# Optimization experiments

Hardware: AMD Instinct MI355X
Metric: run time of the kernel (lower is better)

## Reference

```python
import jax, jax.numpy as jnp
import numpy as np

B, T = 256, 800
D_IN, H, L, V = 128, 512, 2, 128


def setup_inputs() -> dict:
    key = jax.random.key(0)
    ks = jax.random.split(key, 12)
    s = 0.1  # init scale for stability
    return {
        "W_ih0": jax.random.normal(ks[0], (4 * H, D_IN), jnp.float32) * s,
        "W_hh0": jax.random.normal(ks[1], (4 * H, H), jnp.float32) * s,
        "b_ih0": jax.random.normal(ks[2], (4 * H,), jnp.float32) * s,
        "b_hh0": jax.random.normal(ks[3], (4 * H,), jnp.float32) * s,
        "W_ih1": jax.random.normal(ks[4], (4 * H, H), jnp.float32) * s,
        "W_hh1": jax.random.normal(ks[5], (4 * H, H), jnp.float32) * s,
        "b_ih1": jax.random.normal(ks[6], (4 * H,), jnp.float32) * s,
        "b_hh1": jax.random.normal(ks[7], (4 * H,), jnp.float32) * s,
        "W_lin": jax.random.normal(ks[8], (V, H), jnp.float32) * s,
        "b_lin": jax.random.normal(ks[9], (V,), jnp.float32) * s,
        "z": jax.random.randint(ks[10], (B, T), 0, V, jnp.int32),
        "num_frames": jax.random.randint(ks[11], (B,), 100, 800, jnp.int32),
    }


def _lstm_log_prob(layers, W_lin, b_lin, z, num_frames):
    # teacher-forced inputs: step i sees one_hot(z[:, i-1]), zeros at i=0
    oh = jax.nn.one_hot(z[:, :-1], D_IN, dtype=jnp.float32)          # [B, T-1, D]
    inputs = jnp.concatenate([jnp.zeros((B, 1, D_IN), jnp.float32), oh], axis=1)
    inputs = jnp.transpose(inputs, (1, 0, 2))                         # [T, B, D]

    def step(carry, x_t):
        h, c = carry  # each [L, B, H]
        inp = x_t
        hs, cs = [], []
        for l, (Wih, Whh, bih, bhh) in enumerate(layers):
            gates = inp @ Wih.T + h[l] @ Whh.T + bih + bhh            # [B, 4H]
            i, f, g, o = jnp.split(gates, 4, axis=-1)                 # torch gate order i,f,g,o
            c_new = jax.nn.sigmoid(f) * c[l] + jax.nn.sigmoid(i) * jnp.tanh(g)
            h_new = jax.nn.sigmoid(o) * jnp.tanh(c_new)
            hs.append(h_new)
            cs.append(c_new)
            inp = h_new
        logits_t = inp @ W_lin.T + b_lin                              # [B, V]
        return (jnp.stack(hs), jnp.stack(cs)), logits_t

    h0 = jnp.zeros((L, B, H), jnp.float32)
    c0 = jnp.zeros((L, B, H), jnp.float32)
    _, logits = jax.lax.scan(step, (h0, c0), inputs)                  # [T, B, V]
    logits = jnp.transpose(logits, (1, 0, 2))                         # [B, T, V]

    logp = jax.nn.log_softmax(logits, axis=-1)
    nll = -jnp.take_along_axis(logp, z[..., None].astype(jnp.int32), axis=-1)[..., 0]  # [B, T]
    mask = (jnp.arange(T)[None, :] < num_frames[:, None]).astype(nll.dtype)
    return (nll * mask).mean(axis=-1)                                 # [B] (mean over full T, as in torch)


def reference(W_ih0, W_hh0, b_ih0, b_hh0, W_ih1, W_hh1, b_ih1, b_hh1, W_lin, b_lin, z, num_frames):
    layers = [(W_ih0, W_hh0, b_ih0, b_hh0), (W_ih1, W_hh1, b_ih1, b_hh1)]
    return _lstm_log_prob(layers, W_lin, b_lin, z, num_frames)
```

## Files before the change

### kernel.cpp

```cpp
#include <hip/hip_runtime.h>

#define TT 800

typedef __attribute__((ext_vector_type(8))) short bf16x8;
typedef __attribute__((ext_vector_type(4))) float f32x4;
typedef unsigned short u16;
typedef unsigned int u32;
typedef unsigned long long u64;

constexpr int NCW = 128, NWG = 136, RT = 32;
constexpr size_t WL0A_OFF = 0;
constexpr size_t WL0B_OFF = 2097152;
constexpr size_t WL1_OFF  = 2621440;
constexpr size_t WLIN_OFF = 6815744;
constexpr size_t H0_OFF   = 6946816;
constexpr size_t H1_OFF   = 7471104;
constexpr size_t BAR_OFF  = 7995392;
constexpr int HB = 256 * 512;
constexpr int A_ST = 520;
constexpr int G_OFF_B = 33280;
constexpr int P_OFF_B = 49792;
constexpr int LDS_BYTES = 53248;

__device__ __forceinline__ u16 f2b(float x) {
  u32 u = __float_as_uint(x);
  return (u16)((u + 0x7FFFu + ((u >> 16) & 1u)) >> 16);
}
__device__ __forceinline__ float b2f(u16 v) { return __uint_as_float(((u32)v) << 16); }
__device__ __forceinline__ float sigf(float x) { return 1.f / (1.f + __expf(-x)); }
__device__ __forceinline__ float tanh_f(float x) { float e = __expf(2.f * x); return 1.f - 2.f / (e + 1.f); }

__device__ __forceinline__ u64 ld_coh8(const u64* p) {
  return __hip_atomic_load(p, __ATOMIC_RELAXED, __HIP_MEMORY_SCOPE_AGENT);
}
__device__ __forceinline__ void st_coh8(u64* p, u64 v) {
  __hip_atomic_store(p, v, __ATOMIC_RELAXED, __HIP_MEMORY_SCOPE_AGENT);
}
__device__ __forceinline__ void fpost_l(u32* fw, u32 v) {
  *(volatile u32*)fw = v;
}
__device__ __forceinline__ void fpost_a(u32* fw, u32 v) {
  __hip_atomic_store(fw, v, __ATOMIC_RELAXED, __HIP_MEMORY_SCOPE_AGENT);
}
__device__ __forceinline__ void wave_poll(u32* Fw, int lane, u32 thr, bool lok) {
  int idx = (lane < 17) ? lane : 16;
  if (lok) {
    while (true) {
      u32 v = *(volatile u32*)(Fw + idx);
      if (__all((int)(v >= thr))) break;
      asm volatile("buffer_inv" ::: "memory");
    }
  } else {
    while (true) {
      u32 v = __hip_atomic_load(Fw + idx, __ATOMIC_RELAXED, __HIP_MEMORY_SCOPE_AGENT);
      if (__all((int)(v >= thr))) break;
      __builtin_amdgcn_s_sleep(1);
    }
  }
}
__device__ __forceinline__ void l1inv() { asm volatile("buffer_inv" ::: "memory"); }

__global__ void prep_kernel(const float* __restrict__ wih0, const float* __restrict__ whh0,
                            const float* __restrict__ wih1, const float* __restrict__ whh1,
                            const float* __restrict__ wlinf,
                            u16* __restrict__ wl0a, u16* __restrict__ wl0b,
                            u16* __restrict__ wl1, u16* __restrict__ wlin) {
  int i = blockIdx.x * 256 + threadIdx.x;
  const int NA = 2048 * 512, NB = 128 * 2048, N1 = 2048 * 1024, N2 = 128 * 512;
  if (i < NA) {
    int col = i >> 9, k = i & 511;
    wl0a[i] = f2b(whh0[col * 512 + k]);
  } else if (i < NA + NB) {
    int j = i - NA, k = j >> 11, col = j & 2047;
    wl0b[j] = f2b(wih0[col * 128 + k]);
  } else if (i < NA + NB + N1) {
    int j = i - NA - NB, col = j >> 10, k = j & 1023;
    float v = (k < 512) ? wih1[col * 512 + k] : whh1[col * 512 + (k - 512)];
    wl1[j] = f2b(v);
  } else if (i < NA + NB + N1 + N2) {
    int j = i - NA - NB - N1, col = j >> 9, k = j & 511;
    wlin[j] = f2b(wlinf[col * 512 + k]);
  }
}

__global__ __launch_bounds__(256, 1) void lstm_kernel(
    const float* __restrict__ bih0, const float* __restrict__ bhh0,
    const float* __restrict__ bih1, const float* __restrict__ bhh1,
    const float* __restrict__ blin,
    const int* __restrict__ z, const int* __restrict__ nfr,
    const u16* __restrict__ wl0a, const u16* __restrict__ wl0b,
    const u16* __restrict__ wl1, const u16* __restrict__ wlin,
    u16* __restrict__ h0buf, u16* __restrict__ h1buf,
    u32* __restrict__ bars, float* __restrict__ out) {
  extern __shared__ char smem[];
  u16* A = (u16*)smem;
  float* Gf = (float*)(smem + G_OFF_B);
  float* Pm = (float*)(smem + P_OFF_B);
  float* Ps = Pm + 256;
  float* Pt = Ps + 256;
  const int wg = blockIdx.x;
  const int w_all = wg >> 3;
  const bool isC = (w_all < 16);
  const int tile = wg & 7;
  const int w = isC ? w_all : 16;
  const int slot = isC ? w : 16;
  const int tid = threadIdx.x, lane = tid & 63, wv = tid >> 6;
  const int l15 = lane & 15, l4 = lane >> 4;
  const int row0 = tile * RT;
  u32* Fw = bars + tile * 32;
  const f32x4 VZ = {0.f, 0.f, 0.f, 0.f};
  const int rC = tid >> 3, u0C = (tid & 7) * 4;
  const int cuL = tid & 31, rgL = tid >> 5;

  float c0s[4] = {0, 0, 0, 0}, c1s[4] = {0, 0, 0, 0};
  float accN = 0.f, nflv = 0.f;
  float bias0c[2], bias1c[2], biasLc[2];
  bf16x8 bq0R[32];
  bf16x8 bq1R[64];
  bf16x8 wlR[32];

  if (isC) {
#pragma unroll
    for (int cb = 0; cb < 2; ++cb) {
      int col = wv * 512 + w * 32 + cb * 16 + l15;
      bias0c[cb] = bih0[col] + bhh0[col];
      bias1c[cb] = bih1[col] + bhh1[col];
      const u16* b0 = wl0a + (size_t)col * 512 + l4 * 8;
#pragma unroll
      for (int kb = 0; kb < 16; ++kb) bq0R[cb * 16 + kb] = *(const bf16x8*)(b0 + kb * 32);
      const u16* b1 = wl1 + (size_t)col * 1024 + l4 * 8;
#pragma unroll
      for (int kb = 0; kb < 32; ++kb) bq1R[cb * 32 + kb] = *(const bf16x8*)(b1 + kb * 32);
    }
  } else {
#pragma unroll
    for (int cb = 0; cb < 2; ++cb) {
      int colV = wv * 32 + cb * 16 + l15;
      biasLc[cb] = blin[colV];
      const u16* bL = wlin + (size_t)colV * 512 + l4 * 8;
#pragma unroll
      for (int kb = 0; kb < 16; ++kb) wlR[cb * 16 + kb] = *(const bf16x8*)(bL + kb * 32);
    }
    if (rgL == 0) nflv = (float)nfr[row0 + cuL];
  }

  u32 xcc;
  asm volatile("s_getreg_b32 %0, hwreg(HW_REG_XCC_ID)" : "=s"(xcc));
  {
    int* hls = (int*)Pm;
    if (tid == 0) {
      u32 bit = 1u << (xcc & 31u);
      __hip_atomic_fetch_or(bars + 256 + tile, bit, __ATOMIC_RELAXED, __HIP_MEMORY_SCOPE_AGENT);
      __hip_atomic_fetch_add(bars + 272, 1u, __ATOMIC_RELAXED, __HIP_MEMORY_SCOPE_AGENT);
      while (__hip_atomic_load(bars + 272, __ATOMIC_RELAXED, __HIP_MEMORY_SCOPE_AGENT) < (u32)NWG)
        __builtin_amdgcn_s_sleep(1);
      u32 m = __hip_atomic_load(bars + 256 + tile, __ATOMIC_RELAXED, __HIP_MEMORY_SCOPE_AGENT);
      hls[0] = (m == bit) ? 1 : 0;
    }
    __syncthreads();
    const_cast<volatile int&>(hls[0]);
  }
  const bool lok = (((volatile int*)Pm)[0] != 0);
  __syncthreads();

  if (isC && w == 0) {
    u64* z0 = (u64*)(h0buf + HB + row0 * 512);
    u64* z1 = (u64*)(h1buf + row0 * 512);
    u64* z2 = (u64*)(h1buf + HB + row0 * 512);
    if (lok) {
      for (int k = tid; k < 2048; k += 256) { z0[k] = 0; z1[k] = 0; z2[k] = 0; }
    } else {
      for (int k = tid; k < 2048; k += 256) { st_coh8(z0 + k, 0); st_coh8(z1 + k, 0); st_coh8(z2 + k, 0); }
    }
  }
  __syncthreads();
  if (tid == 0) { if (lok) fpost_l(Fw + slot, 1u); else fpost_a(Fw + slot, 1u); }

  auto ldA = [&](int rb, int kb) {
    return *(const bf16x8*)(A + (rb * 16 + l15) * A_ST + kb * 32 + l4 * 8);
  };

#pragma unroll 1
  for (int tau = 0; tau <= TT + 1; ++tau) {
    if (wv == 0) wave_poll(Fw, lane, (u32)(tau + 1), lok);
    __syncthreads();
    if (lok) l1inv();
    const u16* h0src = h0buf + ((tau + 1) & 1) * HB + row0 * 512;
    const u64* h1s64 = (const u64*)(h1buf + (tau & 1) * HB + row0 * 512);
    const bool l0act = isC && (tau < TT);
    const bool l1act = isC && (tau >= 1 && tau <= TT);

    if (isC) {
      if (tau <= TT) {
        u64 ta[8], tb[8];
        const u64* s64 = (const u64*)h0src;
        if (lok) {
#pragma unroll
          for (int c = 0; c < 8; ++c) {
            int li = c * 256 + tid;
            ta[c] = s64[li * 2]; tb[c] = s64[li * 2 + 1];
          }
        } else {
#pragma unroll
          for (int c = 0; c < 8; ++c) {
            int li = c * 256 + tid;
            ta[c] = ld_coh8(s64 + li * 2); tb[c] = ld_coh8(s64 + li * 2 + 1);
          }
        }
#pragma unroll
        for (int c = 0; c < 8; ++c) {
          int li = c * 256 + tid, row = li >> 6, cc = li & 63;
          u64* d = (u64*)(A + row * A_ST + cc * 8);
          d[0] = ta[c]; d[1] = tb[c];
        }
      }
      u64 ha[4], hb[4];
      if (l1act) {
        if (lok) {
#pragma unroll
          for (int c = 0; c < 4; ++c) {
            int li = c * 256 + tid;
            ha[c] = h1s64[li * 2]; hb[c] = h1s64[li * 2 + 1];
          }
        } else {
#pragma unroll
          for (int c = 0; c < 4; ++c) {
            int li = c * 256 + tid;
            ha[c] = ld_coh8(h1s64 + li * 2); hb[c] = ld_coh8(h1s64 + li * 2 + 1);
          }
        }
      }
      __syncthreads();

      f32x4 acc0[2][2] = {{VZ, VZ}, {VZ, VZ}};
      f32x4 acc1[2][2] = {{VZ, VZ}, {VZ, VZ}};
      if (l0act) {
#pragma unroll
        for (int kb = 0; kb < 16; ++kb) {
          bf16x8 a0 = ldA(0, kb), a1 = ldA(1, kb);
#pragma unroll
          for (int cb = 0; cb < 2; ++cb) {
            acc0[0][cb] = __builtin_amdgcn_mfma_f32_16x16x32_bf16(a0, bq0R[cb * 16 + kb], acc0[0][cb], 0, 0, 0);
            acc0[1][cb] = __builtin_amdgcn_mfma_f32_16x16x32_bf16(a1, bq0R[cb * 16 + kb], acc0[1][cb], 0, 0, 0);
          }
        }
      }
      if (l1act) {
#pragma unroll
        for (int kb = 0; kb < 16; ++kb) {
          bf16x8 a0 = ldA(0, kb), a1 = ldA(1, kb);
#pragma unroll
          for (int cb = 0; cb < 2; ++cb) {
            acc1[0][cb] = __builtin_amdgcn_mfma_f32_16x16x32_bf16(a0, bq1R[cb * 32 + kb], acc1[0][cb], 0, 0, 0);
            acc1[1][cb] = __builtin_amdgcn_mfma_f32_16x16x32_bf16(a1, bq1R[cb * 32 + kb], acc1[1][cb], 0, 0, 0);
          }
        }
      }
      if (l0act) {
#pragma unroll
        for (int rb = 0; rb < 2; ++rb)
#pragma unroll
          for (int cb = 0; cb < 2; ++cb)
#pragma unroll
            for (int q = 0; q < 4; ++q)
              Gf[(rb * 16 + l4 * 4 + q) * 129 + wv * 32 + cb * 16 + l15] = acc0[rb][cb][q] + bias0c[cb];
      }
      __syncthreads();

      u64 ha2[4], hb2[4];
      if (l1act) {
        if (lok) {
#pragma unroll
          for (int c = 0; c < 4; ++c) {
            int li = (c + 4) * 256 + tid;
            ha2[c] = h1s64[li * 2]; hb2[c] = h1s64[li * 2 + 1];
          }
        } else {
#pragma unroll
          for (int c = 0; c < 4; ++c) {
            int li = (c + 4) * 256 + tid;
            ha2[c] = ld_coh8(h1s64 + li * 2); hb2[c] = ld_coh8(h1s64 + li * 2 + 1);
          }
        }
      }
      if (l0act) {
        float g4[4][4];
#pragma unroll
        for (int g = 0; g < 4; ++g)
#pragma unroll
          for (int j = 0; j < 4; ++j) g4[g][j] = Gf[rC * 129 + g * 32 + u0C + j];
        if (tau >= 1) {
          int zr = z[(row0 + rC) * TT + (tau - 1)];
          const u16* gb = wl0b + (size_t)zr * 2048 + w * 32 + u0C;
#pragma unroll
          for (int g = 0; g < 4; ++g) {
            u64 v = *(const u64*)(gb + g * 512);
#pragma unroll
            for (int j = 0; j < 4; ++j) g4[g][j] += b2f((u16)(v >> (16 * j)));
          }
        }
        u64 pk = 0;
#pragma unroll
        for (int j = 0; j < 4; ++j) {
          float cn = sigf(g4[1][j]) * c0s[j] + sigf(g4[0][j]) * tanh_f(g4[2][j]);
          float hn = sigf(g4[3][j]) * tanh_f(cn);
          c0s[j] = cn;
          pk |= ((u64)f2b(hn)) << (16 * j);
        }
        u16* h0w = h0buf + (tau & 1) * HB + row0 * 512;
        u64* dst = (u64*)(h0w + rC * 512 + w * 32 + u0C);
        if (lok) *dst = pk; else st_coh8(dst, pk);
      }
      if (l1act) {
#pragma unroll
        for (int c = 0; c < 4; ++c) {
          int li = c * 256 + tid, row = li >> 6, cc = li & 63;
          u64* d = (u64*)(A + row * A_ST + cc * 8);
          d[0] = ha[c]; d[1] = hb[c];
        }
#pragma unroll
        for (int c = 0; c < 4; ++c) {
          int li = (c + 4) * 256 + tid, row = li >> 6, cc = li & 63;
          u64* d = (u64*)(A + row * A_ST + cc * 8);
          d[0] = ha2[c]; d[1] = hb2[c];
        }
      }
      __syncthreads();

      if (l1act) {
#pragma unroll
        for (int kb = 16; kb < 32; ++kb) {
          bf16x8 a0 = ldA(0, kb - 16), a1 = ldA(1, kb - 16);
#pragma unroll
          for (int cb = 0; cb < 2; ++cb) {
            acc1[0][cb] = __builtin_amdgcn_mfma_f32_16x16x32_bf16(a0, bq1R[cb * 32 + kb], acc1[0][cb], 0, 0, 0);
            acc1[1][cb] = __builtin_amdgcn_mfma_f32_16x16x32_bf16(a1, bq1R[cb * 32 + kb], acc1[1][cb], 0, 0, 0);
          }
        }
#pragma unroll
        for (int rb = 0; rb < 2; ++rb)
#pragma unroll
          for (int cb = 0; cb < 2; ++cb)
#pragma unroll
            for (int q = 0; q < 4; ++q)
              Gf[(rb * 16 + l4 * 4 + q) * 129 + wv * 32 + cb * 16 + l15] = acc1[rb][cb][q] + bias1c[cb];
      }
      __syncthreads();

      if (l1act) {
        float g4[4][4];
#pragma unroll
        for (int g = 0; g < 4; ++g)
#pragma unroll
          for (int j = 0; j < 4; ++j) g4[g][j] = Gf[rC * 129 + g * 32 + u0C + j];
        u64 pk = 0;
#pragma unroll
        for (int j = 0; j < 4; ++j) {
          float cn = sigf(g4[1][j]) * c1s[j] + sigf(g4[0][j]) * tanh_f(g4[2][j]);
          float hn = sigf(g4[3][j]) * tanh_f(cn);
          c1s[j] = cn;
          pk |= ((u64)f2b(hn)) << (16 * j);
        }
        u16* h1w = h1buf + ((tau + 1) & 1) * HB + row0 * 512;
        u64* dst = (u64*)(h1w + rC * 512 + w * 32 + u0C);
        if (lok) *dst = pk; else st_coh8(dst, pk);
      }
      __syncthreads();
      if (tid == 0) { if (lok) fpost_l(Fw + slot, (u32)(tau + 2)); else fpost_a(Fw + slot, (u32)(tau + 2)); }
    } else {
      const bool lgact = (tau >= 2);
      if (lgact) {
        u64 ta[8], tb[8];
        if (lok) {
#pragma unroll
          for (int c = 0; c < 8; ++c) {
            int li = c * 256 + tid;
            ta[c] = h1s64[li * 2]; tb[c] = h1s64[li * 2 + 1];
          }
        } else {
#pragma unroll
          for (int c = 0; c < 8; ++c) {
            int li = c * 256 + tid;
            ta[c] = ld_coh8(h1s64 + li * 2); tb[c] = ld_coh8(h1s64 + li * 2 + 1);
          }
        }
#pragma unroll
        for (int c = 0; c < 8; ++c) {
          int li = c * 256 + tid, row = li >> 6, cc = li & 63;
          u64* d = (u64*)(A + row * A_ST + cc * 8);
          d[0] = ta[c]; d[1] = tb[c];
        }
      }
      __syncthreads();
      if (tid == 0) { if (lok) fpost_l(Fw + slot, (u32)(tau + 2)); else fpost_a(Fw + slot, (u32)(tau + 2)); }
      if (lgact) {
        f32x4 accL[2][2] = {{VZ, VZ}, {VZ, VZ}};
#pragma unroll
        for (int kb = 0; kb < 16; ++kb) {
          bf16x8 a0 = ldA(0, kb), a1 = ldA(1, kb);
#pragma unroll
          for (int cb = 0; cb < 2; ++cb) {
            accL[0][cb] = __builtin_amdgcn_mfma_f32_16x16x32_bf16(a0, wlR[cb * 16 + kb], accL[0][cb], 0, 0, 0);
            accL[1][cb] = __builtin_amdgcn_mfma_f32_16x16x32_bf16(a1, wlR[cb * 16 + kb], accL[1][cb], 0, 0, 0);
          }
        }
#pragma unroll
        for (int rb = 0; rb < 2; ++rb)
#pragma unroll
          for (int cb = 0; cb < 2; ++cb)
#pragma unroll
            for (int q = 0; q < 4; ++q)
              Gf[(rb * 16 + l4 * 4 + q) * 129 + wv * 32 + cb * 16 + l15] = accL[rb][cb][q] + biasLc[cb];
      }
      __syncthreads();
      if (lgact) {
        int t2 = tau - 2;
        int r = cuL, k = rgL;
        float vloc[16], mloc = -3.4e38f;
#pragma unroll
        for (int j = 0; j < 16; ++j) {
          vloc[j] = Gf[r * 129 + k * 16 + j];
          mloc = fmaxf(mloc, vloc[j]);
        }
        Pm[r * 8 + k] = mloc;
        __syncthreads();
        float mrow = Pm[r * 8];
#pragma unroll
        for (int j = 1; j < 8; ++j) mrow = fmaxf(mrow, Pm[r * 8 + j]);
        int zr = z[(row0 + r) * TT + t2];
        float sloc = 0.f, tloc = 0.f;
#pragma unroll
        for (int j = 0; j < 16; ++j) {
          sloc += __expf(vloc[j] - mrow);
          tloc += (k * 16 + j == zr) ? vloc[j] : 0.f;
        }
        Ps[r * 8 + k] = sloc; Pt[r * 8 + k] = tloc;
        __syncthreads();
        if (k == 0) {
          float s = 0.f, tv = 0.f;
#pragma unroll
          for (int j = 0; j < 8; ++j) { s += Ps[r * 8 + j]; tv += Pt[r * 8 + j]; }
          if ((float)t2 < nflv) accN += mrow + __logf(s) - tv;
        }
      } else {
        __syncthreads(); __syncthreads();
      }
    }
  }

  if (!isC && rgL == 0) out[row0 + cuL] = accN * (1.0f / TT);
}

extern "C" void kernel_launch(void* const* d_in, const int* in_sizes, int n_in,
                              void* d_out, int out_size, void* d_ws, size_t ws_size,
                              hipStream_t stream) {
  const float* wih0 = (const float*)d_in[0];
  const float* whh0 = (const float*)d_in[1];
  const float* bih0 = (const float*)d_in[2];
  const float* bhh0 = (const float*)d_in[3];
  const float* wih1 = (const float*)d_in[4];
  const float* whh1 = (const float*)d_in[5];
  const float* bih1 = (const float*)d_in[6];
  const float* bhh1 = (const float*)d_in[7];
  const float* wlinf = (const float*)d_in[8];
  const float* blin = (const float*)d_in[9];
  const int* z = (const int*)d_in[10];
  const int* nfr = (const int*)d_in[11];
  float* out = (float*)d_out;
  char* ws = (char*)d_ws;
  u16* wl0a = (u16*)(ws + WL0A_OFF);
  u16* wl0b = (u16*)(ws + WL0B_OFF);
  u16* wl1 = (u16*)(ws + WL1_OFF);
  u16* wlin = (u16*)(ws + WLIN_OFF);
  u16* h0buf = (u16*)(ws + H0_OFF);
  u16* h1buf = (u16*)(ws + H1_OFF);
  u32* bars = (u32*)(ws + BAR_OFF);

  hipMemsetAsync(ws + BAR_OFF, 0, 2048, stream);
  const int NTOT = 2048 * 512 + 128 * 2048 + 2048 * 1024 + 128 * 512;
  prep_kernel<<<dim3((NTOT + 255) / 256), dim3(256), 0, stream>>>(
      wih0, whh0, wih1, whh1, wlinf, wl0a, wl0b, wl1, wlin);
  lstm_kernel<<<dim3(NWG), dim3(256), LDS_BYTES, stream>>>(
      bih0, bhh0, bih1, bhh1, blin, z, nfr, wl0a, wl0b, wl1, wlin, h0buf, h1buf, bars, out);
}
```

Measured before the change: 7.559 ms.

## Use per-wave 16-bit flags and separate LDS buffers to cut per-step barriers

Replaces the per-workgroup step flag, which needed a __syncthreads before polling and before posting, with per-wave 16-bit flags. Every wave now polls four flags per 64-bit load and posts its own flag after an explicit waitcnt. Layer-1 h is staged into a separate LDS buffer A2, and the layer-0 and layer-1 gate buffers are split, so both recurrent matmuls run back to back and two block barriers per step disappear. LDS use roughly doubles, which needs the max-dynamic-shared-memory attribute. Flag-visibility ordering now depends on the per-wave waitcnt rather than a block barrier.

```diff
diff --git a/kernel.cpp b/kernel.cpp
--- a/kernel.cpp
+++ b/kernel.cpp
@@ -8,7 +8,7 @@
 typedef unsigned int u32;
 typedef unsigned long long u64;
 
-constexpr int NCW = 128, NWG = 136, RT = 32;
+constexpr int NWG = 136, RT = 32;
 constexpr size_t WL0A_OFF = 0;
 constexpr size_t WL0B_OFF = 2097152;
 constexpr size_t WL1_OFF  = 2621440;
@@ -18,9 +18,11 @@
 constexpr size_t BAR_OFF  = 7995392;
 constexpr int HB = 256 * 512;
 constexpr int A_ST = 520;
-constexpr int G_OFF_B = 33280;
-constexpr int P_OFF_B = 49792;
-constexpr int LDS_BYTES = 53248;
+constexpr int A2_OFF_B = 33280;
+constexpr int G0_OFF_B = 66560;
+constexpr int G1_OFF_B = 83072;
+constexpr int P_OFF_B  = 99584;
+constexpr int LDS_BYTES = 102656;
 
 __device__ __forceinline__ u16 f2b(float x) {
   u32 u = __float_as_uint(x);
@@ -36,24 +38,23 @@
 __device__ __forceinline__ void st_coh8(u64* p, u64 v) {
   __hip_atomic_store(p, v, __ATOMIC_RELAXED, __HIP_MEMORY_SCOPE_AGENT);
 }
-__device__ __forceinline__ void fpost_l(u32* fw, u32 v) {
-  *(volatile u32*)fw = v;
-}
-__device__ __forceinline__ void fpost_a(u32* fw, u32 v) {
-  __hip_atomic_store(fw, v, __ATOMIC_RELAXED, __HIP_MEMORY_SCOPE_AGENT);
-}
-__device__ __forceinline__ void wave_poll(u32* Fw, int lane, u32 thr, bool lok) {
-  int idx = (lane < 17) ? lane : 16;
+__device__ __forceinline__ void fpost16(u16* fp, u32 v) { *(volatile u16*)fp = (u16)v; }
+__device__ __forceinline__ int f4ok(u64 v, u32 thr) {
+  return ((u32)(v & 0xFFFFu) >= thr) & (((u32)(v >> 16) & 0xFFFFu) >= thr) &
+         (((u32)(v >> 32) & 0xFFFFu) >= thr) & ((u32)(v >> 48) >= thr);
+}
+__device__ __forceinline__ void wave_poll(const u64* F64, int lane, u32 thr, bool lok) {
+  int i = (lane < 17) ? lane : 0;
   if (lok) {
     while (true) {
-      u32 v = *(volatile u32*)(Fw + idx);
-      if (__all((int)(v >= thr))) break;
+      u64 v = *(const volatile u64*)(F64 + i);
+      if (__all(f4ok(v, thr))) break;
       asm volatile("buffer_inv" ::: "memory");
     }
   } else {
     while (true) {
-      u32 v = __hip_atomic_load(Fw + idx, __ATOMIC_RELAXED, __HIP_MEMORY_SCOPE_AGENT);
-      if (__all((int)(v >= thr))) break;
+      u64 v = ld_coh8(F64 + i);
+      if (__all(f4ok(v, thr))) break;
       __builtin_amdgcn_s_sleep(1);
     }
   }
@@ -93,8 +94,10 @@
     u16* __restrict__ h0buf, u16* __restrict__ h1buf,
     u32* __restrict__ bars, float* __restrict__ out) {
   extern __shared__ char smem[];
-  u16* A = (u16*)smem;
-  float* Gf = (float*)(smem + G_OFF_B);
+  u16* A  = (u16*)smem;
+  u16* A2 = (u16*)(smem + A2_OFF_B);
+  float* Gf0 = (float*)(smem + G0_OFF_B);
+  float* Gf1 = (float*)(smem + G1_OFF_B);
   float* Pm = (float*)(smem + P_OFF_B);
   float* Ps = Pm + 256;
   float* Pt = Ps + 256;
@@ -103,11 +106,12 @@
   const bool isC = (w_all < 16);
   const int tile = wg & 7;
   const int w = isC ? w_all : 16;
-  const int slot = isC ? w : 16;
   const int tid = threadIdx.x, lane = tid & 63, wv = tid >> 6;
   const int l15 = lane & 15, l4 = lane >> 4;
   const int row0 = tile * RT;
-  u32* Fw = bars + tile * 32;
+  u16* Fw16 = (u16*)(bars + tile * 64);
+  const u64* F64 = (const u64*)Fw16;
+  const int fslot = isC ? (w * 4 + wv) : (64 + wv);
   const f32x4 VZ = {0.f, 0.f, 0.f, 0.f};
   const int rC = tid >> 3, u0C = (tid & 7) * 4;
   const int cuL = tid & 31, rgL = tid >> 5;
@@ -150,11 +154,11 @@
     int* hls = (int*)Pm;
     if (tid == 0) {
       u32 bit = 1u << (xcc & 31u);
-      __hip_atomic_fetch_or(bars + 256 + tile, bit, __ATOMIC_RELAXED, __HIP_MEMORY_SCOPE_AGENT);
-      __hip_atomic_fetch_add(bars + 272, 1u, __ATOMIC_RELAXED, __HIP_MEMORY_SCOPE_AGENT);
-      while (__hip_atomic_load(bars + 272, __ATOMIC_RELAXED, __HIP_MEMORY_SCOPE_AGENT) < (u32)NWG)
+      __hip_atomic_fetch_or(bars + tile * 64 + 40, bit, __ATOMIC_RELAXED, __HIP_MEMORY_SCOPE_AGENT);
+      __hip_atomic_fetch_add(bars + 48, 1u, __ATOMIC_RELAXED, __HIP_MEMORY_SCOPE_AGENT);
+      while (__hip_atomic_load(bars + 48, __ATOMIC_RELAXED, __HIP_MEMORY_SCOPE_AGENT) < (u32)NWG)
         __builtin_amdgcn_s_sleep(1);
-      u32 m = __hip_atomic_load(bars + 256 + tile, __ATOMIC_RELAXED, __HIP_MEMORY_SCOPE_AGENT);
+      u32 m = __hip_atomic_load(bars + tile * 64 + 40, __ATOMIC_RELAXED, __HIP_MEMORY_SCOPE_AGENT);
       hls[0] = (m == bit) ? 1 : 0;
     }
     __syncthreads();
@@ -174,16 +178,18 @@
     }
   }
   __syncthreads();
-  if (tid == 0) { if (lok) fpost_l(Fw + slot, 1u); else fpost_a(Fw + slot, 1u); }
+  if (lane == 0) fpost16(Fw16 + fslot, 1u);
 
   auto ldA = [&](int rb, int kb) {
     return *(const bf16x8*)(A + (rb * 16 + l15) * A_ST + kb * 32 + l4 * 8);
   };
+  auto ldA2 = [&](int rb, int kb) {
+    return *(const bf16x8*)(A2 + (rb * 16 + l15) * A_ST + kb * 32 + l4 * 8);
+  };
 
 #pragma unroll 1
   for (int tau = 0; tau <= TT + 1; ++tau) {
-    if (wv == 0) wave_poll(Fw, lane, (u32)(tau + 1), lok);
-    __syncthreads();
+    wave_poll(F64, lane, (u32)(tau + 1), lok);
     if (lok) l1inv();
     const u16* h0src = h0buf + ((tau + 1) & 1) * HB + row0 * 512;
     const u64* h1s64 = (const u64*)(h1buf + (tau & 1) * HB + row0 * 512);
@@ -214,8 +220,8 @@
           d[0] = ta[c]; d[1] = tb[c];
         }
       }
-      u64 ha[4], hb[4];
       if (l1act) {
+        u64 ha[4], hb[4];
         if (lok) {
 #pragma unroll
           for (int c = 0; c < 4; ++c) {
@@ -228,6 +234,32 @@
             int li = c * 256 + tid;
             ha[c] = ld_coh8(h1s64 + li * 2); hb[c] = ld_coh8(h1s64 + li * 2 + 1);
           }
+        }
+#pragma unroll
+        for (int c = 0; c < 4; ++c) {
+          int li = c * 256 + tid, row = li >> 6, cc = li & 63;
+          u64* d = (u64*)(A2 + row * A_ST + cc * 8);
+          d[0] = ha[c]; d[1] = hb[c];
+        }
+        u64 ha2[4], hb2[4];
+        if (lok) {
+#pragma unroll
+          for (int c = 0; c < 4; ++c) {
+            int li = (c + 4) * 256 + tid;
+            ha2[c] = h1s64[li * 2]; hb2[c] = h1s64[li * 2 + 1];
+          }
+        } else {
+#pragma unroll
+          for (int c = 0; c < 4; ++c) {
+            int li = (c + 4) * 256 + tid;
+            ha2[c] = ld_coh8(h1s64 + li * 2); hb2[c] = ld_coh8(h1s64 + li * 2 + 1);
+          }
+        }
+#pragma unroll
+        for (int c = 0; c < 4; ++c) {
+          int li = (c + 4) * 256 + tid, row = li >> 6, cc = li & 63;
+          u64* d = (u64*)(A2 + row * A_ST + cc * 8);
+          d[0] = ha2[c]; d[1] = hb2[c];
         }
       }
       __syncthreads();
@@ -255,6 +287,15 @@
             acc1[1][cb] = __builtin_amdgcn_mfma_f32_16x16x32_bf16(a1, bq1R[cb * 32 + kb], acc1[1][cb], 0, 0, 0);
           }
         }
+#pragma unroll
+        for (int kb = 16; kb < 32; ++kb) {
+          bf16x8 a0 = ldA2(0, kb - 16), a1 = ldA2(1, kb - 16);
+#pragma unroll
+          for (int cb = 0; cb < 2; ++cb) {
+            acc1[0][cb] = __builtin_amdgcn_mfma_f32_16x16x32_bf16(a0, bq1R[cb * 32 + kb], acc1[0][cb], 0, 0, 0);
+            acc1[1][cb] = __builtin_amdgcn_mfma_f32_16x16x32_bf16(a1, bq1R[cb * 32 + kb], acc1[1][cb], 0, 0, 0);
+          }
+        }
       }
       if (l0act) {
 #pragma unroll
@@ -263,32 +304,25 @@
           for (int cb = 0; cb < 2; ++cb)
 #pragma unroll
             for (int q = 0; q < 4; ++q)
-              Gf[(rb * 16 + l4 * 4 + q) * 129 + wv * 32 + cb * 16 + l15] = acc0[rb][cb][q] + bias0c[cb];
+              Gf0[(rb * 16 + l4 * 4 + q) * 129 + wv * 32 + cb * 16 + l15] = acc0[rb][cb][q] + bias0c[cb];
+      }
+      if (l1act) {
+#pragma unroll
+        for (int rb = 0; rb < 2; ++rb)
+#pragma unroll
+          for (int cb = 0; cb < 2; ++cb)
+#pragma unroll
+            for (int q = 0; q < 4; ++q)
+              Gf1[(rb * 16 + l4 * 4 + q) * 129 + wv * 32 + cb * 16 + l15] = acc1[rb][cb][q] + bias1c[cb];
       }
       __syncthreads();
 
-      u64 ha2[4], hb2[4];
-      if (l1act) {
-        if (lok) {
-#pragma unroll
-          for (int c = 0; c < 4; ++c) {
-            int li = (c + 4) * 256 + tid;
-            ha2[c] = h1s64[li * 2]; hb2[c] = h1s64[li * 2 + 1];
-          }
-        } else {
-#pragma unroll
-          for (int c = 0; c < 4; ++c) {
-            int li = (c + 4) * 256 + tid;
-            ha2[c] = ld_coh8(h1s64 + li * 2); hb2[c] = ld_coh8(h1s64 + li * 2 + 1);
-          }
-        }
-      }
       if (l0act) {
         float g4[4][4];
 #pragma unroll
         for (int g = 0; g < 4; ++g)
 #pragma unroll
-          for (int j = 0; j < 4; ++j) g4[g][j] = Gf[rC * 129 + g * 32 + u0C + j];
+          for (int j = 0; j < 4; ++j) g4[g][j] = Gf0[rC * 129 + g * 32 + u0C + j];
         if (tau >= 1) {
           int zr = z[(row0 + rC) * TT + (tau - 1)];
           const u16* gb = wl0b + (size_t)zr * 2048 + w * 32 + u0C;
@@ -312,47 +346,11 @@
         if (lok) *dst = pk; else st_coh8(dst, pk);
       }
       if (l1act) {
-#pragma unroll
-        for (int c = 0; c < 4; ++c) {
-          int li = c * 256 + tid, row = li >> 6, cc = li & 63;
-          u64* d = (u64*)(A + row * A_ST + cc * 8);
-          d[0] = ha[c]; d[1] = hb[c];
-        }
-#pragma unroll
-        for (int c = 0; c < 4; ++c) {
-          int li = (c + 4) * 256 + tid, row = li >> 6, cc = li & 63;
-          u64* d = (u64*)(A + row * A_ST + cc * 8);
-          d[0] = ha2[c]; d[1] = hb2[c];
-        }
-      }
-      __syncthreads();
-
-      if (l1act) {
-#pragma unroll
-        for (int kb = 16; kb < 32; ++kb) {
-          bf16x8 a0 = ldA(0, kb - 16), a1 = ldA(1, kb - 16);
-#pragma unroll
-          for (int cb = 0; cb < 2; ++cb) {
-            acc1[0][cb] = __builtin_amdgcn_mfma_f32_16x16x32_bf16(a0, bq1R[cb * 32 + kb], acc1[0][cb], 0, 0, 0);
-            acc1[1][cb] = __builtin_amdgcn_mfma_f32_16x16x32_bf16(a1, bq1R[cb * 32 + kb], acc1[1][cb], 0, 0, 0);
-          }
-        }
-#pragma unroll
-        for (int rb = 0; rb < 2; ++rb)
-#pragma unroll
-          for (int cb = 0; cb < 2; ++cb)
-#pragma unroll
-            for (int q = 0; q < 4; ++q)
-              Gf[(rb * 16 + l4 * 4 + q) * 129 + wv * 32 + cb * 16 + l15] = acc1[rb][cb][q] + bias1c[cb];
-      }
-      __syncthreads();
-
-      if (l1act) {
         float g4[4][4];
 #pragma unroll
         for (int g = 0; g < 4; ++g)
 #pragma unroll
-          for (int j = 0; j < 4; ++j) g4[g][j] = Gf[rC * 129 + g * 32 + u0C + j];
+          for (int j = 0; j < 4; ++j) g4[g][j] = Gf1[rC * 129 + g * 32 + u0C + j];
         u64 pk = 0;
 #pragma unroll
         for (int j = 0; j < 4; ++j) {
@@ -365,8 +363,8 @@
         u64* dst = (u64*)(h1w + rC * 512 + w * 32 + u0C);
         if (lok) *dst = pk; else st_coh8(dst, pk);
       }
-      __syncthreads();
-      if (tid == 0) { if (lok) fpost_l(Fw + slot, (u32)(tau + 2)); else fpost_a(Fw + slot, (u32)(tau + 2)); }
+      asm volatile("s_waitcnt vmcnt(0) lgkmcnt(0)" ::: "memory");
+      if (lane == 0) fpost16(Fw16 + fslot, (u32)(tau + 2));
     } else {
       const bool lgact = (tau >= 2);
       if (lgact) {
@@ -392,7 +390,7 @@
         }
       }
       __syncthreads();
-      if (tid == 0) { if (lok) fpost_l(Fw + slot, (u32)(tau + 2)); else fpost_a(Fw + slot, (u32)(tau + 2)); }
+      if (lane == 0) fpost16(Fw16 + fslot, (u32)(tau + 2));
       if (lgact) {
         f32x4 accL[2][2] = {{VZ, VZ}, {VZ, VZ}};
 #pragma unroll
@@ -410,7 +408,7 @@
           for (int cb = 0; cb < 2; ++cb)
 #pragma unroll
             for (int q = 0; q < 4; ++q)
-              Gf[(rb * 16 + l4 * 4 + q) * 129 + wv * 32 + cb * 16 + l15] = accL[rb][cb][q] + biasLc[cb];
+              Gf0[(rb * 16 + l4 * 4 + q) * 129 + wv * 32 + cb * 16 + l15] = accL[rb][cb][q] + biasLc[cb];
       }
       __syncthreads();
       if (lgact) {
@@ -419,7 +417,7 @@
         float vloc[16], mloc = -3.4e38f;
 #pragma unroll
         for (int j = 0; j < 16; ++j) {
-          vloc[j] = Gf[r * 129 + k * 16 + j];
+          vloc[j] = Gf0[r * 129 + k * 16 + j];
           mloc = fmaxf(mloc, vloc[j]);
         }
         Pm[r * 8 + k] = mloc;
@@ -476,6 +474,13 @@
   u16* h1buf = (u16*)(ws + H1_OFF);
   u32* bars = (u32*)(ws + BAR_OFF);
 
+  static bool attr_set = false;
+  if (!attr_set) {
+    hipFuncSetAttribute(reinterpret_cast<const void*>(lstm_kernel),
+                        hipFuncAttributeMaxDynamicSharedMemorySize, LDS_BYTES);
+    attr_set = true;
+  }
+
   hipMemsetAsync(ws + BAR_OFF, 0, 2048, stream);
   const int NTOT = 2048 * 512 + 128 * 2048 + 2048 * 1024 + 128 * 512;
   prep_kernel<<<dim3((NTOT + 255) / 256), dim3(256), 0, stream>>>(
```

New measurement: 9.404 ms. 1.24x slower.
